# Optimization experiments

Hardware: AMD Instinct MI355X
Metric: run time of the kernel (lower is better)

The kernel has to match this reference:

```python
import jax, jax.numpy as jnp
import numpy as np

# (l, C_l, C_l_TP, C_l_angular) per non-empty l-block of the filter type
FILTER_REPS = [(0, 144, 144, 1), (1, 272, 272, 1), (2, 208, 208, 1), (3, 80, 80, 1), (4, 16, 16, 1)]
FILTER_C = 720      # sum of C_l
FILTER_DIM = 2704   # sum of C_l*(2l+1)
ANG_DIM = 25        # sum of C_l_angular*(2l+1)
DIM_OUT = 52
DIM_IN = 52
Q_OUT, Q_IN, NUM_P = 16, 16, 125
SCALAR_BASIS = 12


def setup_inputs() -> dict:
    key = jax.random.key(0)
    k1, k2, k3, k4, k5 = jax.random.split(key, 5)
    N = Q_OUT * Q_IN * NUM_P
    scalar_kernel_tensor = jax.random.normal(k1, (Q_OUT, Q_IN, NUM_P, SCALAR_BASIS), dtype=jnp.float32)
    angular_kernel_tensor = jax.random.normal(k2, (N, ANG_DIM), dtype=jnp.float32)
    weights = jax.random.normal(k3, (SCALAR_BASIS, FILTER_C), dtype=jnp.float32)
    # TP mixing matrix is a constant sparse buffer (Wigner-3j based); model as sparsified dense
    dense = jax.random.normal(k4, (DIM_OUT * DIM_IN, FILTER_DIM), dtype=jnp.float32)
    mask = jax.random.uniform(k5, (DIM_OUT * DIM_IN, FILTER_DIM)) < 0.05
    TP_mixing = dense * mask.astype(jnp.float32)
    return {"scalar_kernel_tensor": scalar_kernel_tensor,
            "angular_kernel_tensor": angular_kernel_tensor,
            "weights": weights,
            "TP_mixing": TP_mixing}


def mul_scalar_angular(sc, ang):
    # sc: (N, FILTER_C), ang: (N, ANG_DIM) -> (N, FILTER_DIM)
    N = sc.shape[0]
    outs = []
    s = 0
    a = 0
    for (l, C_l, C_l_TP, C_l_ang) in FILTER_REPS:
        m = 2 * l + 1
        dim_ang = C_l_ang * m
        x = (sc[:, s:s + C_l].reshape(N, C_l_ang, C_l_TP, 1)
             * ang[:, a:a + dim_ang].reshape(N, C_l_ang, 1, m))
        outs.append(x.reshape(N, C_l * m))
        s += C_l
        a += dim_ang
    return jnp.concatenate(outs, axis=-1)


def reference(scalar_kernel_tensor, angular_kernel_tensor, weights, TP_mixing):
    N = Q_OUT * Q_IN * NUM_P
    sk = scalar_kernel_tensor.reshape(N, SCALAR_BASIS)
    # combine scalar basis with weights: (N, FILTER_C)
    sc = jnp.einsum('ns,sc->nc', sk, weights / jnp.sqrt(jnp.float32(SCALAR_BASIS)))
    # ragged segment-wise broadcast multiply: (N, FILTER_DIM)
    filt = mul_scalar_angular(sc, angular_kernel_tensor)
    # kernel = (TP_mixing @ filt.T).T == filt @ TP_mixing.T : (N, DIM_OUT*DIM_IN)
    k = filt @ TP_mixing.T
    return k.reshape(Q_OUT, Q_IN, NUM_P, DIM_OUT, DIM_IN)
```

## Files before the change

kernel.cpp:

```cpp
#include <hip/hip_runtime.h>
#include <hip/hip_bf16.h>

#define N_ROWS 32000
#define SB     12
#define FC     720
#define FD     2704
#define OCOLS  2704
#define OPAD   2816
#define ANGD   25
#define PDIM   300
#define KST    320
#define NT     5
#define KP     2720
#define NTV    85
#define GPR    (KP/8)

typedef __attribute__((ext_vector_type(8))) short bf16x8;
typedef __attribute__((ext_vector_type(4))) float f32x4;

__device__ __forceinline__ void gload16(const void* g, void* l) {
    __builtin_amdgcn_global_load_lds(
        (const __attribute__((address_space(1))) void*)g,
        (__attribute__((address_space(3))) void*)l, 16, 0, 0);
}

__device__ __forceinline__ void decode_f(int f, int& c, int& j, int& a) {
    if (f < 144)       { c = f;                         j = 0;            a = 0;  }
    else if (f < 960)  { int t = f - 144;  c = 144 + t/3; j = t - (t/3)*3; a = 1;  }
    else if (f < 2000) { int t = f - 960;  c = 416 + t/5; j = t - (t/5)*5; a = 4;  }
    else if (f < 2560) { int t = f - 2000; c = 624 + t/7; j = t - (t/7)*7; a = 9;  }
    else               { int t = f - 2560; c = 704 + t/9; j = t - (t/9)*9; a = 16; }
}

__global__ void cvt_M(const float* __restrict__ M, __hip_bfloat16* __restrict__ out)
{
    const int g = blockIdx.x * 256 + threadIdx.x;
    if (g >= OPAD * GPR) return;
    const int o = g / GPR;
    const int k = (g - o * GPR) * 8;
    alignas(16) __hip_bfloat16 tmp[8];
    if (o < OCOLS && k + 8 <= FD) {
        const float4* p = (const float4*)(M + (size_t)o * FD + k);
        float4 x0 = p[0], x1 = p[1];
        tmp[0] = __float2bfloat16(x0.x); tmp[1] = __float2bfloat16(x0.y);
        tmp[2] = __float2bfloat16(x0.z); tmp[3] = __float2bfloat16(x0.w);
        tmp[4] = __float2bfloat16(x1.x); tmp[5] = __float2bfloat16(x1.y);
        tmp[6] = __float2bfloat16(x1.z); tmp[7] = __float2bfloat16(x1.w);
    } else {
        #pragma unroll
        for (int u = 0; u < 8; ++u) {
            float v = (o < OCOLS && k + u < FD) ? M[(size_t)o * FD + k + u] : 0.f;
            tmp[u] = __float2bfloat16(v);
        }
    }
    *(bf16x8*)(out + (size_t)o * KP + k) = *(const bf16x8*)tmp;
}

__global__ void build_G(const float* __restrict__ W, __hip_bfloat16* __restrict__ Gt)
{
    const int g = blockIdx.x * 256 + threadIdx.x;
    if (g >= KST * GPR) return;
    const int p  = g / GPR;
    const int f0 = (g - p * GPR) * 8;
    const int s     = p / ANGD;
    const int alpha = p - s * ANGD;
    const float inv = 0.28867513459481288f;
    alignas(16) __hip_bfloat16 tmp[8];
    #pragma unroll
    for (int u = 0; u < 8; ++u) {
        const int f = f0 + u;
        float v = 0.f;
        if (p < PDIM && f < FD) {
            int c, j, a;
            decode_f(f, c, j, a);
            if (alpha == a + j) v = W[s * FC + c] * inv;
        }
        tmp[u] = __float2bfloat16(v);
    }
    *(bf16x8*)(Gt + (size_t)p * KP + f0) = *(const bf16x8*)tmp;
}

__global__ void build_X(const float* __restrict__ sk,
                        const float* __restrict__ ang,
                        __hip_bfloat16* __restrict__ X)
{
    const int idx = blockIdx.x * 256 + threadIdx.x;
    if (idx >= N_ROWS * (KST / 8)) return;
    const int n  = idx / (KST / 8);
    const int p0 = (idx - n * (KST / 8)) * 8;
    const float* skn  = sk  + (size_t)n * SB;
    const float* angn = ang + (size_t)n * ANGD;
    alignas(16) __hip_bfloat16 tmp[8];
    #pragma unroll
    for (int u = 0; u < 8; ++u) {
        const int p = p0 + u;
        float v = 0.f;
        if (p < PDIM) {
            const int s = p / ANGD;
            const int a = p - s * ANGD;
            v = skn[s] * angn[a];
        }
        tmp[u] = __float2bfloat16(v);
    }
    *(bf16x8*)(X + (size_t)n * KST + p0) = *(const bf16x8*)tmp;
}

__global__ __launch_bounds__(256, 4) void gemm_V(
    const __hip_bfloat16* __restrict__ A,
    const __hip_bfloat16* __restrict__ B,
    __hip_bfloat16* __restrict__ V)
{
    __shared__ __align__(1024) char lds[24576];
    char* const bufA = lds;
    char* const bufB = lds + 16384;

    const int tid  = threadIdx.x;
    const int wave = tid >> 6;
    const int lane = tid & 63;

    const int bn = blockIdx.x;
    const int bm = blockIdx.y;
    const size_t arow0 = (size_t)bm * 128;
    const size_t brow0 = (size_t)bn * 64;

    const int wr = wave >> 1;
    const int wc = wave & 1;

    const int lrow2 = lane >> 2;
    const int sslot = (((lane & 3) ^ (lrow2 & 3) ^ ((lane >> 4) & 3))) << 4;

    auto STAGE = [&](int t, int half) {
        char* const la = bufA + half * 8192;
        char* const lb = bufB + half * 4096;
        const char* ga = (const char*)A
            + (arow0 + (size_t)(wave * 16 + lrow2)) * (KP * 2)
            + (size_t)t * 64 + sslot;
        gload16(ga,                         la + wave * 1024);
        gload16(ga + (size_t)64 * (KP * 2), la + 4096 + wave * 1024);
        const char* gb = (const char*)B
            + (brow0 + (size_t)(wave * 16 + lrow2)) * (KP * 2)
            + (size_t)t * 64 + sslot;
        gload16(gb, lb + wave * 1024);
    };

    const int rl   = lane & 15;
    const int koct = lane >> 4;
    const int rslot = ((koct ^ (rl & 3) ^ ((rl >> 2) & 3))) << 4;

    STAGE(0, 0);
    STAGE(1, 1);
    asm volatile("s_waitcnt vmcnt(3)" ::: "memory");
    __builtin_amdgcn_s_barrier();

    f32x4 acc[4][2] = {};

    for (int t = 0; t < NTV; ++t) {
        char* const aC = bufA + (t & 1) * 8192;
        char* const bC = bufB + (t & 1) * 4096;

        bf16x8 af[4], bfr[2];
        #pragma unroll
        for (int m = 0; m < 4; ++m) {
            const int r = wr * 64 + m * 16 + rl;
            af[m] = *(const bf16x8*)(aC + r * 64 + rslot);
        }
        #pragma unroll
        for (int n = 0; n < 2; ++n) {
            const int r = wc * 32 + n * 16 + rl;
            bfr[n] = *(const bf16x8*)(bC + r * 64 + rslot);
        }
        asm volatile("s_waitcnt lgkmcnt(0)" ::: "memory");
        __builtin_amdgcn_sched_barrier(0);
        __builtin_amdgcn_s_barrier();

        if (t + 2 < NTV) STAGE(t + 2, t & 1);

        __builtin_amdgcn_s_setprio(1);
        #pragma unroll
        for (int m = 0; m < 4; ++m)
            #pragma unroll
            for (int n = 0; n < 2; ++n)
                acc[m][n] = __builtin_amdgcn_mfma_f32_16x16x32_bf16(
                    bfr[n], af[m], acc[m][n], 0, 0, 0);
        __builtin_amdgcn_s_setprio(0);
        __builtin_amdgcn_sched_barrier(0);

        if (t < NTV - 2)       asm volatile("s_waitcnt vmcnt(3)" ::: "memory");
        else if (t == NTV - 2) asm volatile("s_waitcnt vmcnt(0)" ::: "memory");
        if (t < NTV - 1) __builtin_amdgcn_s_barrier();
    }

    const int obase = (int)arow0 + wr * 64 + rl;
    const int pbase = (int)brow0 + wc * 32 + koct * 4;
    #pragma unroll
    for (int m = 0; m < 4; ++m) {
        const int orow = obase + m * 16;
        #pragma unroll
        for (int n = 0; n < 2; ++n) {
            const int p = pbase + n * 16;
            alignas(8) __hip_bfloat16 t4[4];
            t4[0] = __float2bfloat16(acc[m][n][0]);
            t4[1] = __float2bfloat16(acc[m][n][1]);
            t4[2] = __float2bfloat16(acc[m][n][2]);
            t4[3] = __float2bfloat16(acc[m][n][3]);
            *(uint2*)(V + (size_t)orow * KST + p) = *(const uint2*)t4;
        }
    }
}

__global__ __launch_bounds__(512, 4) void gemm_bt(
    const __hip_bfloat16* __restrict__ A,
    const __hip_bfloat16* __restrict__ B,
    float* __restrict__ C)
{
    __shared__ __align__(1024) char lds[65536];
    char* const bufA = lds;
    char* const bufB = lds + 32768;
    float* const s_c = (float*)lds;

    const int tid  = threadIdx.x;
    const int wave = tid >> 6;
    const int lane = tid & 63;

    const int bn = blockIdx.x;
    const int bm = blockIdx.y;
    const size_t arow0 = (size_t)bm * 128;
    const size_t brow0 = (size_t)bn * 128;

    const int wr = wave >> 2;
    const int wc = wave & 3;

    const int lrow  = lane >> 3;
    const int lslot = ((lane & 7) ^ (lrow & 7)) << 4;

    auto STAGE = [&](const char* gbase, size_t growbase, int t, char* lbase) {
        const char* g0 = gbase + (growbase + (size_t)(wave * 8 + lrow)) * (KST * 2)
                               + (size_t)t * 128 + lslot;
        gload16(g0,                          lbase + wave * 1024);
        gload16(g0 + (size_t)64 * (KST * 2), lbase + 8192 + wave * 1024);
    };

    const int rl   = lane & 15;
    const int koct = lane >> 4;
    const int sK0 = ((0 * 4 + koct) ^ (lane & 7)) << 4;
    const int sK1 = ((1 * 4 + koct) ^ (lane & 7)) << 4;

    STAGE((const char*)A, arow0, 0, bufA + 0);
    STAGE((const char*)B, brow0, 0, bufB + 0);
    STAGE((const char*)A, arow0, 1, bufA + 16384);
    STAGE((const char*)B, brow0, 1, bufB + 16384);
    asm volatile("s_waitcnt vmcnt(4)" ::: "memory");
    __builtin_amdgcn_s_barrier();

    f32x4 acc[4][2] = {};

    for (int t = 0; t < NT; ++t) {
        char* const aC = bufA + (t & 1) * 16384;
        char* const bC = bufB + (t & 1) * 16384;

        bf16x8 af[4][2], bfr[2][2];
        #pragma unroll
        for (int m = 0; m < 4; ++m) {
            const int r = wr * 64 + m * 16 + rl;
            af[m][0] = *(const bf16x8*)(aC + r * 128 + sK0);
            af[m][1] = *(const bf16x8*)(aC + r * 128 + sK1);
        }
        #pragma unroll
        for (int n = 0; n < 2; ++n) {
            const int r = wc * 32 + n * 16 + rl;
            bfr[n][0] = *(const bf16x8*)(bC + r * 128 + sK0);
            bfr[n][1] = *(const bf16x8*)(bC + r * 128 + sK1);
        }
        asm volatile("s_waitcnt lgkmcnt(0)" ::: "memory");
        __builtin_amdgcn_sched_barrier(0);
        __builtin_amdgcn_s_barrier();

        if (t + 2 < NT) {
            STAGE((const char*)A, arow0, t + 2, aC);
            STAGE((const char*)B, brow0, t + 2, bC);
        }

        __builtin_amdgcn_s_setprio(1);
        #pragma unroll
        for (int ks = 0; ks < 2; ++ks)
            #pragma unroll
            for (int m = 0; m < 4; ++m)
                #pragma unroll
                for (int n = 0; n < 2; ++n)
                    acc[m][n] = __builtin_amdgcn_mfma_f32_16x16x32_bf16(
                        bfr[n][ks], af[m][ks], acc[m][n], 0, 0, 0);
        __builtin_amdgcn_s_setprio(0);
        __builtin_amdgcn_sched_barrier(0);

        if (t < NT - 2)       asm volatile("s_waitcnt vmcnt(4)" ::: "memory");
        else if (t == NT - 2) asm volatile("s_waitcnt vmcnt(0)" ::: "memory");
        if (t < NT - 1) __builtin_amdgcn_s_barrier();
    }

    #pragma unroll
    for (int h = 0; h < 2; ++h) {
        __syncthreads();
        if (wr == h) {
            #pragma unroll
            for (int m = 0; m < 4; ++m) {
                const int row_l = m * 16 + rl;
                #pragma unroll
                for (int n = 0; n < 2; ++n) {
                    const int col = wc * 32 + n * 16 + koct * 4;
                    *(f32x4*)&s_c[row_l * 132 + col] = acc[m][n];
                }
            }
        }
        __syncthreads();
        #pragma unroll
        for (int rr = 0; rr < 4; ++rr) {
            const int idx  = rr * 512 + tid;
            const int row  = idx >> 5;
            const int g4   = (idx & 31) * 4;
            if ((int)brow0 + g4 < OCOLS) {
                const f32x4 v = *(const f32x4*)&s_c[row * 132 + g4];
                __builtin_nontemporal_store(v,
                    (f32x4*)(C + (size_t)(arow0 + h * 64 + row) * OCOLS + brow0 + g4));
            }
        }
    }
}

extern "C" void kernel_launch(void* const* d_in, const int* in_sizes, int n_in,
                              void* d_out, int out_size, void* d_ws, size_t ws_size,
                              hipStream_t stream)
{
    const float* sk  = (const float*)d_in[0];
    const float* ang = (const float*)d_in[1];
    const float* W   = (const float*)d_in[2];
    const float* TP  = (const float*)d_in[3];
    float* out = (float*)d_out;

    __hip_bfloat16* X   = (__hip_bfloat16*)d_ws;
    __hip_bfloat16* Vb  = X   + (size_t)N_ROWS * KST;
    __hip_bfloat16* TPb = Vb  + (size_t)OPAD * KST;
    __hip_bfloat16* Gt  = TPb + (size_t)OPAD * KP;

    cvt_M<<<(OPAD * GPR + 255) / 256, 256, 0, stream>>>(TP, TPb);
    build_G<<<(KST * GPR + 255) / 256, 256, 0, stream>>>(W, Gt);
    build_X<<<(N_ROWS * (KST / 8) + 255) / 256, 256, 0, stream>>>(sk, ang, X);

    dim3 gridV(KST / 64, OPAD / 128);
    gemm_V<<<gridV, 256, 0, stream>>>(TPb, Gt, Vb);

    dim3 grid(OPAD / 128, N_ROWS / 128);
    gemm_bt<<<grid, 512, 0, stream>>>(X, Vb, out);
}
```

Measured before the change: 141.5 us.

## Load GEMM B fragments directly to registers and halve block to 4 waves

The main GEMM now runs 256 threads per block, each wave computing a 64x64 output tile instead of 64x32. The B operand is no longer staged through LDS; each wave loads its B fragments straight from global memory into double-buffered registers one k-step ahead, while A stays on the LDS double-buffered path. This frees about half the LDS and removes the B LDS writes and reads. In exchange, B loads are uncoalesced per-lane 16-byte reads, register pressure roughly doubles, and B reuse across waves now depends on cache rather than shared memory.

```diff
diff --git a/kernel.cpp b/kernel.cpp
--- a/kernel.cpp
+++ b/kernel.cpp
@@ -208,14 +208,13 @@
     }
 }
 
-__global__ __launch_bounds__(512, 4) void gemm_bt(
+__global__ __launch_bounds__(256, 2) void gemm_bt(
     const __hip_bfloat16* __restrict__ A,
     const __hip_bfloat16* __restrict__ B,
     float* __restrict__ C)
 {
-    __shared__ __align__(1024) char lds[65536];
+    __shared__ __align__(1024) char lds[34816];
     char* const bufA = lds;
-    char* const bufB = lds + 32768;
     float* const s_c = (float*)lds;
 
     const int tid  = threadIdx.x;
@@ -227,17 +226,19 @@
     const size_t arow0 = (size_t)bm * 128;
     const size_t brow0 = (size_t)bn * 128;
 
-    const int wr = wave >> 2;
-    const int wc = wave & 3;
+    const int wr = wave >> 1;
+    const int wc = wave & 1;
 
     const int lrow  = lane >> 3;
     const int lslot = ((lane & 7) ^ (lrow & 7)) << 4;
-
-    auto STAGE = [&](const char* gbase, size_t growbase, int t, char* lbase) {
-        const char* g0 = gbase + (growbase + (size_t)(wave * 8 + lrow)) * (KST * 2)
-                               + (size_t)t * 128 + lslot;
-        gload16(g0,                          lbase + wave * 1024);
-        gload16(g0 + (size_t)64 * (KST * 2), lbase + 8192 + wave * 1024);
+    auto STAGE_A = [&](int t, char* lbase) {
+        const char* g0 = (const char*)A
+            + (arow0 + (size_t)(wave * 8 + lrow)) * (KST * 2)
+            + (size_t)t * 128 + lslot;
+        #pragma unroll
+        for (int ps = 0; ps < 4; ++ps)
+            gload16(g0 + (size_t)(32 * ps) * (KST * 2),
+                    lbase + ps * 4096 + wave * 1024);
     };
 
     const int rl   = lane & 15;
@@ -245,40 +246,47 @@
     const int sK0 = ((0 * 4 + koct) ^ (lane & 7)) << 4;
     const int sK1 = ((1 * 4 + koct) ^ (lane & 7)) << 4;
 
-    STAGE((const char*)A, arow0, 0, bufA + 0);
-    STAGE((const char*)B, brow0, 0, bufB + 0);
-    STAGE((const char*)A, arow0, 1, bufA + 16384);
-    STAGE((const char*)B, brow0, 1, bufB + 16384);
+    const char* const Bb = (const char*)B;
+    auto LOADB = [&](int t, bf16x8 (&dst)[4][2]) {
+        #pragma unroll
+        for (int n = 0; n < 4; ++n) {
+            const char* bp = Bb
+                + (brow0 + (size_t)(wc * 64 + n * 16 + rl)) * (KST * 2)
+                + (size_t)t * 128 + koct * 16;
+            dst[n][0] = *(const bf16x8*)(bp);
+            dst[n][1] = *(const bf16x8*)(bp + 64);
+        }
+    };
+
+    bf16x8 bEven[4][2], bOdd[4][2];
+    STAGE_A(0, bufA + 0);
+    LOADB(0, bEven);
+    STAGE_A(1, bufA + 16384);
     asm volatile("s_waitcnt vmcnt(4)" ::: "memory");
     __builtin_amdgcn_s_barrier();
 
-    f32x4 acc[4][2] = {};
-
+    f32x4 acc[4][4] = {};
+
+    #pragma unroll
     for (int t = 0; t < NT; ++t) {
         char* const aC = bufA + (t & 1) * 16384;
-        char* const bC = bufB + (t & 1) * 16384;
-
-        bf16x8 af[4][2], bfr[2][2];
+        bf16x8 (&bcur)[4][2] = (t & 1) ? bOdd : bEven;
+        bf16x8 (&bnxt)[4][2] = (t & 1) ? bEven : bOdd;
+
+        if (t + 1 < NT) LOADB(t + 1, bnxt);
+
+        bf16x8 af[4][2];
         #pragma unroll
         for (int m = 0; m < 4; ++m) {
             const int r = wr * 64 + m * 16 + rl;
             af[m][0] = *(const bf16x8*)(aC + r * 128 + sK0);
             af[m][1] = *(const bf16x8*)(aC + r * 128 + sK1);
         }
-        #pragma unroll
-        for (int n = 0; n < 2; ++n) {
-            const int r = wc * 32 + n * 16 + rl;
-            bfr[n][0] = *(const bf16x8*)(bC + r * 128 + sK0);
-            bfr[n][1] = *(const bf16x8*)(bC + r * 128 + sK1);
-        }
         asm volatile("s_waitcnt lgkmcnt(0)" ::: "memory");
         __builtin_amdgcn_sched_barrier(0);
         __builtin_amdgcn_s_barrier();
 
-        if (t + 2 < NT) {
-            STAGE((const char*)A, arow0, t + 2, aC);
-            STAGE((const char*)B, brow0, t + 2, bC);
-        }
+        if (t + 2 < NT) STAGE_A(t + 2, aC);
 
         __builtin_amdgcn_s_setprio(1);
         #pragma unroll
@@ -286,9 +294,9 @@
             #pragma unroll
             for (int m = 0; m < 4; ++m)
                 #pragma unroll
-                for (int n = 0; n < 2; ++n)
+                for (int n = 0; n < 4; ++n)
                     acc[m][n] = __builtin_amdgcn_mfma_f32_16x16x32_bf16(
-                        bfr[n][ks], af[m][ks], acc[m][n], 0, 0, 0);
+                        bcur[n][ks], af[m][ks], acc[m][n], 0, 0, 0);
         __builtin_amdgcn_s_setprio(0);
         __builtin_amdgcn_sched_barrier(0);
 
@@ -305,18 +313,18 @@
             for (int m = 0; m < 4; ++m) {
                 const int row_l = m * 16 + rl;
                 #pragma unroll
-                for (int n = 0; n < 2; ++n) {
-                    const int col = wc * 32 + n * 16 + koct * 4;
+                for (int n = 0; n < 4; ++n) {
+                    const int col = wc * 64 + n * 16 + koct * 4;
                     *(f32x4*)&s_c[row_l * 132 + col] = acc[m][n];
                 }
             }
         }
         __syncthreads();
         #pragma unroll
-        for (int rr = 0; rr < 4; ++rr) {
-            const int idx  = rr * 512 + tid;
-            const int row  = idx >> 5;
-            const int g4   = (idx & 31) * 4;
+        for (int rr = 0; rr < 8; ++rr) {
+            const int idx = rr * 256 + tid;
+            const int row = idx >> 5;
+            const int g4  = (idx & 31) * 4;
             if ((int)brow0 + g4 < OCOLS) {
                 const f32x4 v = *(const f32x4*)&s_c[row * 132 + g4];
                 __builtin_nontemporal_store(v,
@@ -349,5 +357,5 @@
     gemm_V<<<gridV, 256, 0, stream>>>(TPb, Gt, Vb);
 
     dim3 grid(OPAD / 128, N_ROWS / 128);
-    gemm_bt<<<grid, 512, 0, stream>>>(X, Vb, out);
-}
+    gemm_bt<<<grid, 256, 0, stream>>>(X, Vb, out);
+}
```

After: 190.5 us. 34.6% more time.

## Keep A row-panel resident in registers and stream B column tiles per block

Applied to the files above, without the earlier changes.

The final GEMM now gives each block a 128-row panel of X with the full K=320. That panel is loaded once into LDS and then into registers. The block loops over 43 column tiles of 64 from V, double-buffering the B tiles, and writes each output tile through LDS with regular instead of nontemporal stores. This removes the repeated A reloads of the 2D grid, but it shrinks the grid to 250 blocks, raises register use (af holds 40 vectors) and LDS to 114KB, and halves occupancy.

```diff
diff --git a/kernel.cpp b/kernel.cpp
--- a/kernel.cpp
+++ b/kernel.cpp
@@ -10,7 +10,7 @@
 #define ANGD   25
 #define PDIM   300
 #define KST    320
-#define NT     5
+#define NCIT   43
 #define KP     2720
 #define NTV    85
 #define GPR    (KP/8)
@@ -208,119 +208,117 @@
     }
 }
 
-__global__ __launch_bounds__(512, 4) void gemm_bt(
+__global__ __launch_bounds__(512, 2) void gemm_bt(
     const __hip_bfloat16* __restrict__ A,
-    const __hip_bfloat16* __restrict__ B,
+    const __hip_bfloat16* __restrict__ Bv,
     float* __restrict__ C)
 {
-    __shared__ __align__(1024) char lds[65536];
-    char* const bufA = lds;
-    char* const bufB = lds + 32768;
-    float* const s_c = (float*)lds;
+    __shared__ __align__(1024) char lds[116736];
 
     const int tid  = threadIdx.x;
     const int wave = tid >> 6;
     const int lane = tid & 63;
-
-    const int bn = blockIdx.x;
-    const int bm = blockIdx.y;
+    const int bm   = blockIdx.x;
     const size_t arow0 = (size_t)bm * 128;
-    const size_t brow0 = (size_t)bn * 128;
 
     const int wr = wave >> 2;
     const int wc = wave & 3;
 
     const int lrow  = lane >> 3;
     const int lslot = ((lane & 7) ^ (lrow & 7)) << 4;
-
-    auto STAGE = [&](const char* gbase, size_t growbase, int t, char* lbase) {
-        const char* g0 = gbase + (growbase + (size_t)(wave * 8 + lrow)) * (KST * 2)
-                               + (size_t)t * 128 + lslot;
-        gload16(g0,                          lbase + wave * 1024);
-        gload16(g0 + (size_t)64 * (KST * 2), lbase + 8192 + wave * 1024);
-    };
-
     const int rl   = lane & 15;
     const int koct = lane >> 4;
     const int sK0 = ((0 * 4 + koct) ^ (lane & 7)) << 4;
     const int sK1 = ((1 * 4 + koct) ^ (lane & 7)) << 4;
 
-    STAGE((const char*)A, arow0, 0, bufA + 0);
-    STAGE((const char*)B, brow0, 0, bufB + 0);
-    STAGE((const char*)A, arow0, 1, bufA + 16384);
-    STAGE((const char*)B, brow0, 1, bufB + 16384);
-    asm volatile("s_waitcnt vmcnt(4)" ::: "memory");
+    float* const s_c = (float*)(lds + 81920);
+
+    #pragma unroll
+    for (int kt = 0; kt < 5; ++kt) {
+        const char* g0 = (const char*)A
+            + (arow0 + (size_t)(wave * 8 + lrow)) * (KST * 2)
+            + (size_t)kt * 128 + lslot;
+        gload16(g0,                          lds + kt * 16384 + wave * 1024);
+        gload16(g0 + (size_t)64 * (KST * 2), lds + kt * 16384 + 8192 + wave * 1024);
+    }
+    asm volatile("s_waitcnt vmcnt(0)" ::: "memory");
     __builtin_amdgcn_s_barrier();
 
-    f32x4 acc[4][2] = {};
-
-    for (int t = 0; t < NT; ++t) {
-        char* const aC = bufA + (t & 1) * 16384;
-        char* const bC = bufB + (t & 1) * 16384;
-
-        bf16x8 af[4][2], bfr[2][2];
+    bf16x8 af[4][10];
+    #pragma unroll
+    for (int kt = 0; kt < 5; ++kt)
         #pragma unroll
         for (int m = 0; m < 4; ++m) {
             const int r = wr * 64 + m * 16 + rl;
-            af[m][0] = *(const bf16x8*)(aC + r * 128 + sK0);
-            af[m][1] = *(const bf16x8*)(aC + r * 128 + sK1);
-        }
-        #pragma unroll
-        for (int n = 0; n < 2; ++n) {
-            const int r = wc * 32 + n * 16 + rl;
-            bfr[n][0] = *(const bf16x8*)(bC + r * 128 + sK0);
-            bfr[n][1] = *(const bf16x8*)(bC + r * 128 + sK1);
-        }
-        asm volatile("s_waitcnt lgkmcnt(0)" ::: "memory");
-        __builtin_amdgcn_sched_barrier(0);
-        __builtin_amdgcn_s_barrier();
-
-        if (t + 2 < NT) {
-            STAGE((const char*)A, arow0, t + 2, aC);
-            STAGE((const char*)B, brow0, t + 2, bC);
-        }
-
-        __builtin_amdgcn_s_setprio(1);
-        #pragma unroll
-        for (int ks = 0; ks < 2; ++ks)
+            af[m][2 * kt]     = *(const bf16x8*)(lds + kt * 16384 + r * 128 + sK0);
+            af[m][2 * kt + 1] = *(const bf16x8*)(lds + kt * 16384 + r * 128 + sK1);
+        }
+    asm volatile("s_waitcnt lgkmcnt(0)" ::: "memory");
+    __builtin_amdgcn_sched_barrier(0);
+    __builtin_amdgcn_s_barrier();
+
+    auto STAGE_B = [&](int ct, int half) {
+        const char* g0 = (const char*)Bv
+            + ((size_t)ct * 64 + (size_t)(wave * 8 + lrow)) * (KST * 2) + lslot;
+        #pragma unroll
+        for (int kk = 0; kk < 5; ++kk)
+            gload16(g0 + (size_t)kk * 128,
+                    lds + half * 40960 + kk * 8192 + wave * 1024);
+    };
+
+    STAGE_B(0, 0);
+    asm volatile("s_waitcnt vmcnt(0)" ::: "memory");
+    __builtin_amdgcn_s_barrier();
+
+    const int brl  = wc * 16 + rl;
+    const int colw = wc * 16 + koct * 4;
+
+    for (int t = 0; t < NCIT; ++t) {
+        const int half = t & 1;
+        if (t + 1 < NCIT) STAGE_B(t + 1, half ^ 1);
+
+        f32x4 acc[4] = {};
+        char* const bh = lds + half * 40960;
+        #pragma unroll
+        for (int kk = 0; kk < 5; ++kk) {
+            const bf16x8 b0 = *(const bf16x8*)(bh + kk * 8192 + brl * 128 + sK0);
+            const bf16x8 b1 = *(const bf16x8*)(bh + kk * 8192 + brl * 128 + sK1);
             #pragma unroll
             for (int m = 0; m < 4; ++m)
-                #pragma unroll
-                for (int n = 0; n < 2; ++n)
-                    acc[m][n] = __builtin_amdgcn_mfma_f32_16x16x32_bf16(
-                        bfr[n][ks], af[m][ks], acc[m][n], 0, 0, 0);
-        __builtin_amdgcn_s_setprio(0);
-        __builtin_amdgcn_sched_barrier(0);
-
-        if (t < NT - 2)       asm volatile("s_waitcnt vmcnt(4)" ::: "memory");
-        else if (t == NT - 2) asm volatile("s_waitcnt vmcnt(0)" ::: "memory");
-        if (t < NT - 1) __builtin_amdgcn_s_barrier();
-    }
-
-    #pragma unroll
-    for (int h = 0; h < 2; ++h) {
+                acc[m] = __builtin_amdgcn_mfma_f32_16x16x32_bf16(
+                    b0, af[m][2 * kk], acc[m], 0, 0, 0);
+            #pragma unroll
+            for (int m = 0; m < 4; ++m)
+                acc[m] = __builtin_amdgcn_mfma_f32_16x16x32_bf16(
+                    b1, af[m][2 * kk + 1], acc[m], 0, 0, 0);
+        }
+
+        #pragma unroll
+        for (int m = 0; m < 4; ++m)
+            *(f32x4*)&s_c[(wr * 64 + m * 16 + rl) * 68 + colw] = acc[m];
         __syncthreads();
-        if (wr == h) {
-            #pragma unroll
-            for (int m = 0; m < 4; ++m) {
-                const int row_l = m * 16 + rl;
-                #pragma unroll
-                for (int n = 0; n < 2; ++n) {
-                    const int col = wc * 32 + n * 16 + koct * 4;
-                    *(f32x4*)&s_c[row_l * 132 + col] = acc[m][n];
+        const int o0 = t * 64;
+        if (t < NCIT - 1) {
+            #pragma unroll
+            for (int r4 = 0; r4 < 4; ++r4) {
+                const int idx = r4 * 512 + tid;
+                const int row = idx >> 4;
+                const int g4  = (idx & 15) * 4;
+                const f32x4 v = *(const f32x4*)&s_c[row * 68 + g4];
+                *(f32x4*)(C + (size_t)(arow0 + row) * OCOLS + o0 + g4) = v;
+            }
+            asm volatile("s_waitcnt vmcnt(4)" ::: "memory");
+            __builtin_amdgcn_s_barrier();
+        } else {
+            #pragma unroll
+            for (int r4 = 0; r4 < 4; ++r4) {
+                const int idx = r4 * 512 + tid;
+                const int row = idx >> 4;
+                const int g4  = (idx & 15) * 4;
+                if (o0 + g4 < OCOLS) {
+                    const f32x4 v = *(const f32x4*)&s_c[row * 68 + g4];
+                    *(f32x4*)(C + (size_t)(arow0 + row) * OCOLS + o0 + g4) = v;
                 }
-            }
-        }
-        __syncthreads();
-        #pragma unroll
-        for (int rr = 0; rr < 4; ++rr) {
-            const int idx  = rr * 512 + tid;
-            const int row  = idx >> 5;
-            const int g4   = (idx & 31) * 4;
-            if ((int)brow0 + g4 < OCOLS) {
-                const f32x4 v = *(const f32x4*)&s_c[row * 132 + g4];
-                __builtin_nontemporal_store(v,
-                    (f32x4*)(C + (size_t)(arow0 + h * 64 + row) * OCOLS + brow0 + g4));
             }
         }
     }
@@ -348,6 +346,5 @@
     dim3 gridV(KST / 64, OPAD / 128);
     gemm_V<<<gridV, 256, 0, stream>>>(TPb, Gt, Vb);
 
-    dim3 grid(OPAD / 128, N_ROWS / 128);
-    gemm_bt<<<grid, 512, 0, stream>>>(X, Vb, out);
-}
+    gemm_bt<<<N_ROWS / 128, 512, 0, stream>>>(X, Vb, out);
+}
```

Result: slower. 147.4 us (+4.2%).
